# Kernel optimization log

Measured on AMD Instinct MI355X. Metric: run time of the kernel, lower is better.

## Reference

```python
import jax, jax.numpy as jnp
import numpy as np

NUM_BITS = 16           # continuousVarEncodingNumBits
THRESH = 4.0            # segmentActivationThreshold
K_SYN = 32              # numberOfSynapsesPerSegment
B, F, H, C = 512, 128, 8192, 10
E = F * NUM_BITS        # encodedFeatureSize = 2048


def _make_weight(key, n, p):
    # Dense int8-style weights: ~K_SYN random +/-1 synapses per neuron, rest 0.
    k1, k2 = jax.random.split(key)
    signs = jnp.where(jax.random.bernoulli(k1, 0.5, (n, p)), 1.0, -1.0)
    mask = jax.random.bernoulli(k2, K_SYN / p, (n, p))
    return (signs * mask).astype(jnp.float32)


def setup_inputs() -> dict:
    key = jax.random.key(0)
    ks = jax.random.split(key, 6)
    x = jax.random.uniform(ks[0], (B, F), dtype=jnp.float32)
    W0 = _make_weight(ks[1], H, E)   # layer 0: hidden x encoded
    W1 = _make_weight(ks[2], H, H)
    W2 = _make_weight(ks[3], H, H)
    # output connection matrix (numberOfHiddenLayers, hidden, classes); float variant
    outConn = jax.random.uniform(ks[4], (3, H, C), dtype=jnp.float32)
    return {"trainOrTest": 0, "x": x, "W0": W0, "W1": W1, "W2": W2, "outConn": outConn}


def reference(trainOrTest, x, W0, W1, W2, outConn):
    # thermometer bit-encoding of continuous vars: bit j on if x*NUM_BITS > j
    levels = jnp.arange(NUM_BITS, dtype=x.dtype)
    bits = jnp.where(x[:, :, None] * NUM_BITS > levels, 1.0, 0.0)  # (B, F, NUM_BITS)
    act = bits.reshape(x.shape[0], -1).astype(jnp.float32)          # (B, E)

    outAct = jnp.zeros((x.shape[0], outConn.shape[-1]), dtype=jnp.float32)
    for i, W in enumerate((W0, W1, W2)):
        z = act @ W.T                                   # segment sums (B, H)
        act = jnp.where(z >= THRESH, 1.0, 0.0)          # binary segment activation
        outAct = outAct + jnp.einsum('bh,hc->bc', act, outConn[i])
    preds = jnp.argmax(outAct, axis=-1)
    return preds, outAct
```

## Files before the change

### kernel.cpp

```cpp
#include <hip/hip_runtime.h>
#include <stdint.h>

#define BATCH   512
#define NFEAT   128
#define ESIZE   2048
#define HSIZE   8192
#define NCLS    10
#define THRESH_I 4
#define CAP     128
#define ROWB    64


__global__ __launch_bounds__(256) void encode_kernel(
    const float* __restrict__ x,
    uint8_t* __restrict__ aT0, uint8_t* __restrict__ aT1,
    uint8_t* __restrict__ aT2, uint8_t* __restrict__ aT3,
    float* __restrict__ outAcc) {
  int t = blockIdx.x * 256 + threadIdx.x;
  if (t < BATCH * NCLS) outAcc[t] = 0.0f;
  else if (t < 5120 + 64)  aT0[(size_t)ESIZE * ROWB + (t - 5120)] = 0;
  else if (t < 5184 + 64)  aT1[(size_t)HSIZE * ROWB + (t - 5184)] = 0;
  else if (t < 5248 + 64)  aT2[(size_t)HSIZE * ROWB + (t - 5248)] = 0;
  else if (t < 5312 + 64)  aT3[(size_t)HSIZE * ROWB + (t - 5312)] = 0;

  int wave = threadIdx.x >> 6;
  int lane = threadIdx.x & 63;
  int f = blockIdx.x * 4 + wave;
  if (f < NFEAT) {
    float u[8];
#pragma unroll
    for (int i = 0; i < 8; ++i)
      u[i] = x[(size_t)(lane + 64 * i) * NFEAT + f] * 16.0f;
#pragma unroll
    for (int j = 0; j < 16; ++j) {
      uint32_t byte = 0;
#pragma unroll
      for (int i = 0; i < 8; ++i)
        byte |= (u[i] > (float)j ? 1u : 0u) << i;
      aT0[(size_t)(f * 16 + j) * ROWB + lane] = (uint8_t)byte;
    }
  }
}

__global__ __launch_bounds__(256, 8) void convert_kernel(
    const float* __restrict__ W0, const float* __restrict__ W1,
    const float* __restrict__ W2,
    uint32_t* __restrict__ lists, int* __restrict__ counts) {
  int wid = (blockIdx.x * 256 + threadIdx.x) >> 6;
  int lane = threadIdx.x & 63;
  const float* W;
  int row, P;
  if (wid < HSIZE)            { W = W0; row = wid;             P = ESIZE; }
  else if (wid < 2 * HSIZE)   { W = W1; row = wid - HSIZE;     P = HSIZE; }
  else                        { W = W2; row = wid - 2 * HSIZE; P = HSIZE; }

  const float4* w4 = (const float4*)(W + (size_t)row * P);
  uint32_t* lp = lists + (size_t)wid * CAP;
  uint64_t lmask = (lane == 0) ? 0ull : (~0ull >> (64 - lane));
  int nit = P >> 9;
  int cnt = 0;
  float4 c0 = w4[lane];
  float4 c1 = w4[64 + lane];

  for (int it = 0; it < nit; ++it) {
    float4 n0, n1;
    bool more = (it + 1 < nit);
    if (more) {
      n0 = w4[(it + 1) * 128 + lane];
      n1 = w4[(it + 1) * 128 + 64 + lane];
    }
    float v[8] = {c0.x, c0.y, c0.z, c0.w, c1.x, c1.y, c1.z, c1.w};
    uint64_t m[8];
    int tt[8];
#pragma unroll
    for (int k = 0; k < 8; ++k) {
      m[k] = __ballot(v[k] != 0.0f);
      tt[k] = (int)__popcll(m[k]);
    }
    int off = cnt;
#pragma unroll
    for (int k = 0; k < 8; ++k) {
      if (v[k] != 0.0f) {
        int pos = off + (int)__popcll(m[k] & lmask);
        int e = it * 512 + (k >> 2) * 256 + (k & 3) + lane * 4;
        if (pos < CAP)
          lp[pos] = ((uint32_t)e << 1) | (v[k] < 0.0f ? 1u : 0u);
      }
      off += tt[k];
    }
    cnt = off;
    if (more) { c0 = n0; c1 = n1; }
  }
  int pad = (8 - (cnt & 7)) & 7;
  if (lane < pad && cnt + lane < CAP) lp[cnt + lane] = (uint32_t)(P << 1);
  if (lane == 0) counts[wid] = (cnt + pad <= CAP) ? (cnt + pad) : -1;
}

__device__ __forceinline__ void proc_ent(uint32_t ent,
                                         const uint8_t* __restrict__ aIn,
                                         int lane, int* z) {
  uint32_t negm = (uint32_t)(-(int)(ent & 1u));
  uint32_t ee = ent >> 1;
  uint32_t byte = (uint32_t)aIn[(size_t)ee * ROWB + lane];
#pragma unroll
  for (int i = 0; i < 8; ++i) {
    uint32_t t = (byte >> i) & 1u;
    z[i] += (int)((t ^ negm) - negm);
  }
}

__device__ __forceinline__ void proc_comp_dense(float v, int ebase,
                                                const uint8_t* __restrict__ aIn,
                                                int lane, int* z) {
  uint64_t m = __ballot(v != 0.0f);
  if (m == 0ull) return;
  uint64_t pm = __ballot(v > 0.0f);
  do {
    uint32_t src = (uint32_t)__builtin_ctzll(m);
    m &= m - 1;
    int e = ebase + 4 * (int)src;
    uint32_t negm = ((pm >> src) & 1ull) ? 0u : 0xFFFFFFFFu;
    uint32_t byte = (uint32_t)aIn[(size_t)e * ROWB + lane];
#pragma unroll
    for (int i = 0; i < 8; ++i) {
      uint32_t t = (byte >> i) & 1u;
      z[i] += (int)((t ^ negm) - negm);
    }
  } while (m);
}

template <int P>
__global__ __launch_bounds__(512, 4) void layer_kernel(
    const uint32_t* __restrict__ lists, const int* __restrict__ counts,
    const float* __restrict__ W,
    const uint8_t* __restrict__ aIn, uint8_t* __restrict__ aOut) {
  int wave = threadIdx.x >> 6;
  int lane = threadIdx.x & 63;
  int hbase = blockIdx.x * 16 + wave * 2;

  for (int r = 0; r < 2; ++r) {
    int h = hbase + r;
    int z[8];
#pragma unroll
    for (int i = 0; i < 8; ++i) z[i] = 0;

    int cnt = counts[h];
    if (cnt >= 0) {
      const uint32_t* lp = lists + (size_t)h * CAP;
      if (cnt > 0) {
        uint4 eA = *(const uint4*)(lp);
        uint4 eB = *(const uint4*)(lp + 4);
        for (int i = 0; i < cnt; i += 8) {
          uint4 nA = *(const uint4*)(lp + i + 8);
          uint4 nB = *(const uint4*)(lp + i + 12);
          proc_ent(eA.x, aIn, lane, z);
          proc_ent(eA.y, aIn, lane, z);
          proc_ent(eA.z, aIn, lane, z);
          proc_ent(eA.w, aIn, lane, z);
          proc_ent(eB.x, aIn, lane, z);
          proc_ent(eB.y, aIn, lane, z);
          proc_ent(eB.z, aIn, lane, z);
          proc_ent(eB.w, aIn, lane, z);
          eA = nA;
          eB = nB;
        }
      }
    } else {
      const float4* wrow = (const float4*)(W + (size_t)h * P) + lane;
      for (int it = 0; it < P / 256; ++it) {
        float4 wv = wrow[it * 64];
        int eb = it * 256;
        proc_comp_dense(wv.x, eb + 0, aIn, lane, z);
        proc_comp_dense(wv.y, eb + 1, aIn, lane, z);
        proc_comp_dense(wv.z, eb + 2, aIn, lane, z);
        proc_comp_dense(wv.w, eb + 3, aIn, lane, z);
      }
    }

    uint32_t ob = 0;
#pragma unroll
    for (int i = 0; i < 8; ++i)
      ob |= (z[i] >= THRESH_I ? 1u : 0u) << i;
    aOut[(size_t)h * ROWB + lane] = (uint8_t)ob;
  }
}

#define OCHUNK 128
__global__ __launch_bounds__(256, 4) void outacc_kernel(
    const float* __restrict__ outConn,
    const uint8_t* __restrict__ a1, const uint8_t* __restrict__ a2,
    const uint8_t* __restrict__ a3,
    float* __restrict__ outAcc) {
  __shared__ float shOC[OCHUNK][NCLS];
  __shared__ float shAcc[BATCH * NCLS];
  int tid = threadIdx.x;
  int gbase = blockIdx.x * OCHUNK;
  for (int idx = tid; idx < OCHUNK * NCLS; idx += 256)
    ((float*)shOC)[idx] = outConn[(size_t)gbase * NCLS + idx];
  for (int idx = tid; idx < BATCH * NCLS; idx += 256) shAcc[idx] = 0.0f;
  __syncthreads();

  int wave = tid >> 6;
  int lane = tid & 63;
  int layer = gbase >> 13;
  const uint8_t* aT = (layer == 0) ? a1 : (layer == 1) ? a2 : a3;
  int h0 = (gbase & (HSIZE - 1)) + wave * 32;

  float acc[8][NCLS];
#pragma unroll
  for (int i = 0; i < 8; ++i)
#pragma unroll
    for (int c = 0; c < NCLS; ++c) acc[i][c] = 0.0f;

  for (int r = 0; r < 32; ++r) {
    int row = h0 + r;
    uint32_t byte = (uint32_t)aT[(size_t)row * ROWB + lane];
    float bf[8];
#pragma unroll
    for (int i = 0; i < 8; ++i) bf[i] = (float)((byte >> i) & 1u);
    const float* oc = shOC[wave * 32 + r];
#pragma unroll
    for (int c = 0; c < NCLS; ++c) {
      float o = oc[c];
#pragma unroll
      for (int i = 0; i < 8; ++i) acc[i][c] += bf[i] * o;
    }
  }
#pragma unroll
  for (int i = 0; i < 8; ++i)
#pragma unroll
    for (int c = 0; c < NCLS; ++c)
      atomicAdd(&shAcc[(size_t)(lane + 64 * i) * NCLS + c], acc[i][c]);
  __syncthreads();
  for (int idx = tid; idx < BATCH * NCLS; idx += 256)
    atomicAdd(&outAcc[idx], shAcc[idx]);
}

__global__ __launch_bounds__(256) void final_kernel(
    const float* __restrict__ outAcc,
    int* __restrict__ preds,
    float* __restrict__ outF) {
  int b = blockIdx.x * 256 + threadIdx.x;
  if (b < BATCH) {
    float vals[NCLS];
#pragma unroll
    for (int c = 0; c < NCLS; ++c) vals[c] = outAcc[b * NCLS + c];
    float best = vals[0];
    int bi = 0;
#pragma unroll
    for (int c = 1; c < NCLS; ++c) {
      if (vals[c] > best) { best = vals[c]; bi = c; }
    }
    preds[b] = bi;
#pragma unroll
    for (int c = 0; c < NCLS; ++c) outF[b * NCLS + c] = vals[c];
  }
}

extern "C" void kernel_launch(void* const* d_in, const int* in_sizes, int n_in,
                              void* d_out, int out_size, void* d_ws, size_t ws_size,
                              hipStream_t stream) {
  const float* x       = (const float*)d_in[1];
  const float* W0      = (const float*)d_in[2];
  const float* W1      = (const float*)d_in[3];
  const float* W2      = (const float*)d_in[4];
  const float* outConn = (const float*)d_in[5];

  uint8_t* base = (uint8_t*)d_ws;
  uint8_t* aT0 = base;
  uint8_t* aT1 = base + 0x40000;
  uint8_t* aT2 = aT1 + 0x90000;
  uint8_t* aT3 = aT2 + 0x90000;
  uint32_t* lists = (uint32_t*)(aT3 + 0x90000);
  int* counts = (int*)((uint8_t*)lists + (size_t)3 * HSIZE * CAP * 4);
  float* outAcc = (float*)(counts + 3 * HSIZE);

  encode_kernel<<<32, 256, 0, stream>>>(x, aT0, aT1, aT2, aT3, outAcc);
  convert_kernel<<<6144, 256, 0, stream>>>(W0, W1, W2, lists, counts);
  layer_kernel<ESIZE><<<512, 512, 0, stream>>>(
      lists, counts, W0, aT0, aT1);
  layer_kernel<HSIZE><<<512, 512, 0, stream>>>(
      lists + (size_t)HSIZE * CAP, counts + HSIZE, W1, aT1, aT2);
  layer_kernel<HSIZE><<<512, 512, 0, stream>>>(
      lists + (size_t)2 * HSIZE * CAP, counts + 2 * HSIZE, W2, aT2, aT3);
  outacc_kernel<<<192, 256, 0, stream>>>(outConn, aT1, aT2, aT3, outAcc);
  final_kernel<<<2, 256, 0, stream>>>(outAcc, (int*)d_out,
                                      (float*)d_out + BATCH);
}
```

Before: 659.3 us.

## Parallelize weight-to-list conversion across row segments with atomic slot reservation

The conversion kernel previously used one wave per weight row, walking the whole row serially. Now each wave handles a 1024-element segment (two 512 chunks) and reserves its output positions in the row's sparse list with an atomicAdd on the count. This gives many more waves in flight to stream the dense weights. The layer kernel handles the resulting unpadded counts with a masked tail, and uses count > CAP instead of -1 to select the dense fallback. Entry order within a list becomes nondeterministic, and the counts must now be zeroed in the encode kernel.

```diff
diff --git a/kernel.cpp b/kernel.cpp
--- a/kernel.cpp
+++ b/kernel.cpp
@@ -15,6 +15,7 @@
     const float* __restrict__ x,
     uint8_t* __restrict__ aT0, uint8_t* __restrict__ aT1,
     uint8_t* __restrict__ aT2, uint8_t* __restrict__ aT3,
+    int* __restrict__ counts,
     float* __restrict__ outAcc) {
   int t = blockIdx.x * 256 + threadIdx.x;
   if (t < BATCH * NCLS) outAcc[t] = 0.0f;
@@ -22,6 +23,9 @@
   else if (t < 5184 + 64)  aT1[(size_t)HSIZE * ROWB + (t - 5184)] = 0;
   else if (t < 5248 + 64)  aT2[(size_t)HSIZE * ROWB + (t - 5248)] = 0;
   else if (t < 5312 + 64)  aT3[(size_t)HSIZE * ROWB + (t - 5312)] = 0;
+  counts[t] = 0;
+  counts[t + 8192] = 0;
+  counts[t + 16384] = 0;
 
   int wave = threadIdx.x >> 6;
   int lane = threadIdx.x & 63;
@@ -46,54 +50,63 @@
     const float* __restrict__ W0, const float* __restrict__ W1,
     const float* __restrict__ W2,
     uint32_t* __restrict__ lists, int* __restrict__ counts) {
-  int wid = (blockIdx.x * 256 + threadIdx.x) >> 6;
+  int pair = (blockIdx.x * 256 + threadIdx.x) >> 6;
   int lane = threadIdx.x & 63;
+
   const float* W;
-  int row, P;
-  if (wid < HSIZE)            { W = W0; row = wid;             P = ESIZE; }
-  else if (wid < 2 * HSIZE)   { W = W1; row = wid - HSIZE;     P = HSIZE; }
-  else                        { W = W2; row = wid - 2 * HSIZE; P = HSIZE; }
-
-  const float4* w4 = (const float4*)(W + (size_t)row * P);
-  uint32_t* lp = lists + (size_t)wid * CAP;
-  uint64_t lmask = (lane == 0) ? 0ull : (~0ull >> (64 - lane));
-  int nit = P >> 9;
-  int cnt = 0;
+  int row, sloc, wid, P;
+  if (pair < 16384) {
+    W = W0; P = ESIZE;
+    int s0 = pair * 2;
+    row = s0 >> 2; sloc = s0 & 3; wid = row;
+  } else if (pair < 16384 + 65536) {
+    W = W1; P = HSIZE;
+    int s0 = (pair - 16384) * 2;
+    row = s0 >> 4; sloc = s0 & 15; wid = HSIZE + row;
+  } else {
+    W = W2; P = HSIZE;
+    int s0 = (pair - 16384 - 65536) * 2;
+    row = s0 >> 4; sloc = s0 & 15; wid = 2 * HSIZE + row;
+  }
+
+  const float4* w4 = (const float4*)(W + (size_t)row * P + (size_t)sloc * 512);
   float4 c0 = w4[lane];
   float4 c1 = w4[64 + lane];
-
-  for (int it = 0; it < nit; ++it) {
-    float4 n0, n1;
-    bool more = (it + 1 < nit);
-    if (more) {
-      n0 = w4[(it + 1) * 128 + lane];
-      n1 = w4[(it + 1) * 128 + 64 + lane];
-    }
-    float v[8] = {c0.x, c0.y, c0.z, c0.w, c1.x, c1.y, c1.z, c1.w};
-    uint64_t m[8];
-    int tt[8];
-#pragma unroll
-    for (int k = 0; k < 8; ++k) {
-      m[k] = __ballot(v[k] != 0.0f);
-      tt[k] = (int)__popcll(m[k]);
-    }
-    int off = cnt;
-#pragma unroll
-    for (int k = 0; k < 8; ++k) {
-      if (v[k] != 0.0f) {
-        int pos = off + (int)__popcll(m[k] & lmask);
-        int e = it * 512 + (k >> 2) * 256 + (k & 3) + lane * 4;
-        if (pos < CAP)
-          lp[pos] = ((uint32_t)e << 1) | (v[k] < 0.0f ? 1u : 0u);
-      }
-      off += tt[k];
-    }
-    cnt = off;
-    if (more) { c0 = n0; c1 = n1; }
-  }
-  int pad = (8 - (cnt & 7)) & 7;
-  if (lane < pad && cnt + lane < CAP) lp[cnt + lane] = (uint32_t)(P << 1);
-  if (lane == 0) counts[wid] = (cnt + pad <= CAP) ? (cnt + pad) : -1;
+  float4 c2 = w4[128 + lane];
+  float4 c3 = w4[192 + lane];
+
+  float v[16] = {c0.x, c0.y, c0.z, c0.w, c1.x, c1.y, c1.z, c1.w,
+                 c2.x, c2.y, c2.z, c2.w, c3.x, c3.y, c3.z, c3.w};
+  uint64_t m[16];
+  int tt[16];
+#pragma unroll
+  for (int k = 0; k < 16; ++k) {
+    m[k] = __ballot(v[k] != 0.0f);
+    tt[k] = (int)__popcll(m[k]);
+  }
+  int total = 0;
+#pragma unroll
+  for (int k = 0; k < 16; ++k) total += tt[k];
+  if (total == 0) return;
+
+  int base = 0;
+  if (lane == 0) base = atomicAdd(&counts[wid], total);
+  base = __shfl(base, 0);
+
+  uint64_t lmask = (lane == 0) ? 0ull : (~0ull >> (64 - lane));
+  int ebase = sloc * 512;
+  uint32_t* lp = lists + (size_t)wid * CAP;
+  int off = base;
+#pragma unroll
+  for (int k = 0; k < 16; ++k) {
+    if (v[k] != 0.0f) {
+      int pos = off + (int)__popcll(m[k] & lmask);
+      int e = ebase + (k >> 2) * 256 + (k & 3) + lane * 4;
+      if (pos < CAP)
+        lp[pos] = ((uint32_t)e << 1) | (v[k] < 0.0f ? 1u : 0u);
+    }
+    off += tt[k];
+  }
 }
 
 __device__ __forceinline__ void proc_ent(uint32_t ent,
@@ -137,6 +150,7 @@
   int wave = threadIdx.x >> 6;
   int lane = threadIdx.x & 63;
   int hbase = blockIdx.x * 16 + wave * 2;
+  const uint32_t SENT = (uint32_t)(P << 1);
 
   for (int r = 0; r < 2; ++r) {
     int h = hbase + r;
@@ -145,25 +159,30 @@
     for (int i = 0; i < 8; ++i) z[i] = 0;
 
     int cnt = counts[h];
-    if (cnt >= 0) {
+    if (cnt <= CAP) {
       const uint32_t* lp = lists + (size_t)h * CAP;
-      if (cnt > 0) {
-        uint4 eA = *(const uint4*)(lp);
-        uint4 eB = *(const uint4*)(lp + 4);
-        for (int i = 0; i < cnt; i += 8) {
-          uint4 nA = *(const uint4*)(lp + i + 8);
-          uint4 nB = *(const uint4*)(lp + i + 12);
-          proc_ent(eA.x, aIn, lane, z);
-          proc_ent(eA.y, aIn, lane, z);
-          proc_ent(eA.z, aIn, lane, z);
-          proc_ent(eA.w, aIn, lane, z);
-          proc_ent(eB.x, aIn, lane, z);
-          proc_ent(eB.y, aIn, lane, z);
-          proc_ent(eB.z, aIn, lane, z);
-          proc_ent(eB.w, aIn, lane, z);
-          eA = nA;
-          eB = nB;
-        }
+      int full = cnt & ~7;
+      for (int i = 0; i < full; i += 8) {
+        uint4 eA = *(const uint4*)(lp + i);
+        uint4 eB = *(const uint4*)(lp + i + 4);
+        proc_ent(eA.x, aIn, lane, z);
+        proc_ent(eA.y, aIn, lane, z);
+        proc_ent(eA.z, aIn, lane, z);
+        proc_ent(eA.w, aIn, lane, z);
+        proc_ent(eB.x, aIn, lane, z);
+        proc_ent(eB.y, aIn, lane, z);
+        proc_ent(eB.z, aIn, lane, z);
+        proc_ent(eB.w, aIn, lane, z);
+      }
+      if (cnt & 7) {
+        uint4 eA = *(const uint4*)(lp + full);
+        uint4 eB = *(const uint4*)(lp + full + 4);
+        uint32_t ee[8] = {eA.x, eA.y, eA.z, eA.w, eB.x, eB.y, eB.z, eB.w};
+#pragma unroll
+        for (int j = 0; j < 8; ++j)
+          ee[j] = (full + j < cnt) ? ee[j] : SENT;
+#pragma unroll
+        for (int j = 0; j < 8; ++j) proc_ent(ee[j], aIn, lane, z);
       }
     } else {
       const float4* wrow = (const float4*)(W + (size_t)h * P) + lane;
@@ -272,11 +291,12 @@
   uint8_t* aT2 = aT1 + 0x90000;
   uint8_t* aT3 = aT2 + 0x90000;
   uint32_t* lists = (uint32_t*)(aT3 + 0x90000);
-  int* counts = (int*)((uint8_t*)lists + (size_t)3 * HSIZE * CAP * 4);
+  int* counts = (int*)((uint8_t*)lists +
+                       ((size_t)3 * HSIZE * CAP + 64) * 4);
   float* outAcc = (float*)(counts + 3 * HSIZE);
 
-  encode_kernel<<<32, 256, 0, stream>>>(x, aT0, aT1, aT2, aT3, outAcc);
-  convert_kernel<<<6144, 256, 0, stream>>>(W0, W1, W2, lists, counts);
+  encode_kernel<<<32, 256, 0, stream>>>(x, aT0, aT1, aT2, aT3, counts, outAcc);
+  convert_kernel<<<36864, 256, 0, stream>>>(W0, W1, W2, lists, counts);
   layer_kernel<ESIZE><<<512, 512, 0, stream>>>(
       lists, counts, W0, aT0, aT1);
   layer_kernel<HSIZE><<<512, 512, 0, stream>>>(
```

Measured after the change: 651.4 us. About the same (-1.2%).
